# Performance work log

Hardware: AMD Instinct MI355X
Metric: run time of the kernel (lower is better)

The kernel has to match this reference:

```python
import jax, jax.numpy as jnp
import numpy as np

B, T, E, H = 1, 4096, 768, 12
DH = E // H


def setup_inputs() -> dict:
    key = jax.random.key(0)
    ks = jax.random.split(key, 10)
    s = 0.02
    inp = {
        "queries": jax.random.normal(ks[0], (B, T, E), jnp.float32),
        "values": jax.random.normal(ks[1], (B, T, E), jnp.float32),
        # causal mask (1 = keep, 0 = masked), matches masked_fill(mask == 0, -1e9)
        "mask": jnp.tril(jnp.ones((T, T), jnp.int32))[None, None, :, :],
        "Wq": jax.random.normal(ks[2], (E, E), jnp.float32) * s,
        "bq": jnp.zeros((E,), jnp.float32),
        "Wk": jax.random.normal(ks[3], (E, E), jnp.float32) * s,
        "bk": jnp.zeros((E,), jnp.float32),
        "Wv": jax.random.normal(ks[4], (E, E), jnp.float32) * s,
        "bv": jnp.zeros((E,), jnp.float32),
        "Wo": jax.random.normal(ks[5], (E, E), jnp.float32) * s,
        "bo": jnp.zeros((E,), jnp.float32),
    }
    return inp


def _split_heads(x):
    # [B,T,E] -> [B,H,T,DH]
    return x.reshape(B, T, H, DH).transpose(0, 2, 1, 3)


def reference(queries, values, mask, Wq, bq, Wk, bk, Wv, bv, Wo, bo):
    # torch nn.Linear: y = x @ W.T + b
    q = _split_heads(queries @ Wq.T + bq)
    k = _split_heads(values @ Wk.T + bk)
    v = _split_heads(values @ Wv.T + bv)
    scale = 1.0 / np.sqrt(DH).astype(np.float32)
    logits = jnp.einsum("bhqd,bhkd->bhqk", q, k) * scale  # [B,H,T,T]
    logits = jnp.where(mask == 0, jnp.float32(-1e9), logits)
    probs = jax.nn.softmax(logits, axis=-1)
    ctx = jnp.einsum("bhqk,bhkd->bhqd", probs, v)  # [B,H,T,DH]
    ctx = ctx.transpose(0, 2, 1, 3).reshape(B, T, E)
    return ctx @ Wo.T + bo
```

## Files before the change

kernel.cpp:

```cpp
#include <hip/hip_runtime.h>
#include <hip/hip_bf16.h>


typedef __hip_bfloat16 bf16;
typedef __attribute__((ext_vector_type(8))) short short8;
typedef __attribute__((ext_vector_type(4))) short short4v;
typedef __attribute__((ext_vector_type(4))) float f32x4;

#define TSEQ 4096
#define NHEAD 12
#define DHEAD 64
#define EMB 768

#if defined(__HIP_DEVICE_COMPILE__)
#define MFMA16(a, b, c) __builtin_amdgcn_mfma_f32_16x16x16bf16_1k(a, b, c, 0, 0, 0)
#else
#define MFMA16(a, b, c) (c)
#endif

typedef const __attribute__((address_space(1))) unsigned int* gptr_t;
typedef __attribute__((address_space(3))) unsigned int* lptr_t;

__device__ __forceinline__ void load_lds16(const void* g, void* l) {
    __builtin_amdgcn_global_load_lds((gptr_t)g, (lptr_t)l, 16, 0, 0);
}

__device__ __forceinline__ float b2f(short s) {
    unsigned u = ((unsigned)(unsigned short)s) << 16;
    float f;
    __builtin_memcpy(&f, &u, 4);
    return f;
}

__device__ __forceinline__ short f2bs(float f) {
    bf16 h = __float2bfloat16(f);
    short s;
    __builtin_memcpy(&s, &h, 2);
    return s;
}

struct CvtJob { const float* src; bf16* dst; int n; };
struct CvtArgs { CvtJob j[6]; };

__global__ __launch_bounds__(256) void cvt_kernel(CvtArgs a) {
    const CvtJob jb = a.j[blockIdx.y];
    const int i = (blockIdx.x * 256 + threadIdx.x) * 8;
    if (i >= jb.n) return;
    const float4 x0 = *(const float4*)(jb.src + i);
    const float4 x1 = *(const float4*)(jb.src + i + 4);
    bf16 tmp[8];
    tmp[0] = __float2bfloat16(x0.x); tmp[1] = __float2bfloat16(x0.y);
    tmp[2] = __float2bfloat16(x0.z); tmp[3] = __float2bfloat16(x0.w);
    tmp[4] = __float2bfloat16(x1.x); tmp[5] = __float2bfloat16(x1.y);
    tmp[6] = __float2bfloat16(x1.z); tmp[7] = __float2bfloat16(x1.w);
    *(short8*)(jb.dst + i) = *(const short8*)tmp;
}

template<int NF>
__device__ __forceinline__ void gemm_t(
    const bf16* __restrict__ A, const bf16* __restrict__ W,
    const float* __restrict__ bias,
    bf16* __restrict__ outb, float* __restrict__ outf,
    const int mode, const float scale, const int m0, const int n0,
    bf16* sA, bf16* sB)
{
    const int tid  = threadIdx.x;
    const int lane = tid & 63;
    const int wave = tid >> 6;
    const int wr = wave >> 1, wc = wave & 1;
    const int lg = lane >> 4, lr = lane & 15;

    f32x4 acc[4][NF];
#pragma unroll
    for (int m = 0; m < 4; ++m)
#pragma unroll
        for (int n = 0; n < NF; ++n)
            acc[m][n] = (f32x4){0.f, 0.f, 0.f, 0.f};

    for (int k0 = 0; k0 < EMB; k0 += 64) {
        if (k0) __syncthreads();
#pragma unroll
        for (int is = 0; is < 4; ++is) {
            const int chunk = is * 256 + tid;
            const int row = chunk >> 3;
            const int csw = (chunk & 7) ^ (row & 7);
            load_lds16(A + (size_t)(m0 + row) * EMB + k0 + csw * 8,
                       sA + is * 2048 + wave * 512);
        }
#pragma unroll
        for (int is = 0; is < NF; ++is) {
            const int chunk = is * 256 + tid;
            const int row = chunk >> 3;
            const int csw = (chunk & 7) ^ (row & 7);
            load_lds16(W + (size_t)(n0 + row) * EMB + k0 + csw * 8,
                       sB + is * 2048 + wave * 512);
        }
        __syncthreads();

        short8 af[4][2], bfv[NF][2];
#pragma unroll
        for (int m = 0; m < 4; ++m)
#pragma unroll
            for (int kk = 0; kk < 2; ++kk) {
                const int row = wr * 64 + m * 16 + lr;
                const int cc = (kk * 4 + lg) ^ (row & 7);
                af[m][kk] = *(const short8*)(sA + row * 64 + cc * 8);
            }
#pragma unroll
        for (int n = 0; n < NF; ++n)
#pragma unroll
            for (int kk = 0; kk < 2; ++kk) {
                const int row = wc * (NF * 16) + n * 16 + lr;
                const int cc = (kk * 4 + lg) ^ (row & 7);
                bfv[n][kk] = *(const short8*)(sB + row * 64 + cc * 8);
            }
#pragma unroll
        for (int kk = 0; kk < 2; ++kk)
#pragma unroll
            for (int m = 0; m < 4; ++m)
#pragma unroll
                for (int n = 0; n < NF; ++n)
                    acc[m][n] = __builtin_amdgcn_mfma_f32_16x16x32_bf16(
                        af[m][kk], bfv[n][kk], acc[m][n], 0, 0, 0);
    }

#pragma unroll
    for (int n = 0; n < NF; ++n) {
        const int o = n0 + wc * (NF * 16) + n * 16 + lr;
        const float bv = bias[o];
#pragma unroll
        for (int m = 0; m < 4; ++m) {
            const int tbase = m0 + wr * 64 + m * 16 + lg * 4;
#pragma unroll
            for (int r = 0; r < 4; ++r) {
                const float v = (acc[m][n][r] + bv) * scale;
                const int t = tbase + r;
                if (mode == 0)
                    outb[(size_t)(o >> 6) * TSEQ * DHEAD + (size_t)t * DHEAD + (o & 63)] =
                        __float2bfloat16(v);
                else if (mode == 1)
                    outb[(size_t)(o >> 6) * DHEAD * TSEQ + (size_t)(o & 63) * TSEQ + t] =
                        __float2bfloat16(v);
                else
                    outf[(size_t)t * EMB + o] = v;
            }
        }
    }
}

struct QkvArgs {
    const bf16 *xq, *xv, *Wq, *Wk, *Wv;
    const float *bq, *bk, *bv;
    bf16 *qo, *ko, *vto;
};

__global__ __launch_bounds__(256) void qkv_gemm(QkvArgs a) {
    __shared__ __attribute__((aligned(16))) bf16 sA[128 * 64];
    __shared__ __attribute__((aligned(16))) bf16 sB[64 * 64];
    const int z = blockIdx.z;
    const bf16* A = (z == 0) ? a.xq : a.xv;
    const bf16* W = (z == 0) ? a.Wq : (z == 1 ? a.Wk : a.Wv);
    const float* b = (z == 0) ? a.bq : (z == 1 ? a.bk : a.bv);
    bf16* o = (z == 0) ? a.qo : (z == 1 ? a.ko : a.vto);
    const int mode = (z == 2) ? 1 : 0;
    const float scale = (z == 0) ? 0.18033688011112042f : 1.0f;
    gemm_t<2>(A, W, b, o, nullptr, mode, scale, blockIdx.x * 128, blockIdx.y * 64, sA, sB);
}

__global__ __launch_bounds__(256) void out_gemm(
    const bf16* __restrict__ ctx, const bf16* __restrict__ Wo,
    const float* __restrict__ bo, float* __restrict__ out)
{
    __shared__ __attribute__((aligned(16))) bf16 sA[128 * 64];
    __shared__ __attribute__((aligned(16))) bf16 sB[64 * 64];
    gemm_t<2>(ctx, Wo, bo, nullptr, out, 2, 1.0f, blockIdx.x * 128, blockIdx.y * 64, sA, sB);
}

struct AttnState {
    f32x4 O[4];
    float m, l;
};

__device__ __forceinline__ void stage_tile(
    const bf16* __restrict__ Kh, const bf16* __restrict__ Vh,
    bf16* sK, bf16* sV, const int kv0, const int tid)
{
    const int wave = tid >> 6;
#pragma unroll
    for (int is = 0; is < 2; ++is) {
        const int chunk = is * 256 + tid;
        const int row = chunk >> 3;
        const int csw = (chunk & 7) ^ (row & 7);
        load_lds16(Kh + (size_t)(kv0 + row) * DHEAD + csw * 8,
                   sK + is * 2048 + wave * 512);
        load_lds16(Vh + (size_t)row * TSEQ + kv0 + csw * 8,
                   sV + is * 2048 + wave * 512);
    }
}

__device__ __forceinline__ void attn_tile(
    const bf16* sK, const bf16* sV,
    const short8 (&qf)[2], AttnState& st,
    const int kv0, const int qw, const int lane)
{
    const int lg = lane >> 4, lr = lane & 15;
    if (kv0 > qw + 15) return;

    f32x4 s[4];
#pragma unroll
    for (int n = 0; n < 4; ++n) s[n] = (f32x4){0.f, 0.f, 0.f, 0.f};
    short8 kf[4][2];
#pragma unroll
    for (int n = 0; n < 4; ++n)
#pragma unroll
        for (int kk = 0; kk < 2; ++kk) {
            const int row = n * 16 + lr;
            const int cc = (kk * 4 + lg) ^ (row & 7);
            kf[n][kk] = *(const short8*)(sK + row * 64 + cc * 8);
        }
#pragma unroll
    for (int kk = 0; kk < 2; ++kk)
#pragma unroll
        for (int n = 0; n < 4; ++n)
            s[n] = __builtin_amdgcn_mfma_f32_16x16x32_bf16(
                kf[n][kk], qf[kk], s[n], 0, 0, 0);

    if (kv0 + 63 > qw) {
        const int qi = qw + lr;
#pragma unroll
        for (int n = 0; n < 4; ++n) {
            const int kb = kv0 + n * 16 + lg * 4;
#pragma unroll
            for (int r = 0; r < 4; ++r)
                if (kb + r > qi) s[n][r] = -3.0e38f;
        }
    }

    const float a0 = fmaxf(fmaxf(s[0][0], s[0][1]), fmaxf(s[0][2], s[0][3]));
    const float a1 = fmaxf(fmaxf(s[1][0], s[1][1]), fmaxf(s[1][2], s[1][3]));
    const float a2 = fmaxf(fmaxf(s[2][0], s[2][1]), fmaxf(s[2][2], s[2][3]));
    const float a3 = fmaxf(fmaxf(s[3][0], s[3][1]), fmaxf(s[3][2], s[3][3]));
    float mx = fmaxf(fmaxf(a0, a1), fmaxf(a2, a3));
    mx = fmaxf(mx, __shfl_xor(mx, 16));
    mx = fmaxf(mx, __shfl_xor(mx, 32));

    const float mn = fmaxf(st.m, mx);
    const float al = __builtin_amdgcn_exp2f(st.m - mn);
    st.m = mn;

    float rsn[4];
    short4v pq[4];
#pragma unroll
    for (int n = 0; n < 4; ++n) {
        const float p0 = __builtin_amdgcn_exp2f(s[n][0] - mn);
        const float p1 = __builtin_amdgcn_exp2f(s[n][1] - mn);
        const float p2 = __builtin_amdgcn_exp2f(s[n][2] - mn);
        const float p3 = __builtin_amdgcn_exp2f(s[n][3] - mn);
        rsn[n] = (p0 + p1) + (p2 + p3);
        pq[n][0] = f2bs(p0); pq[n][1] = f2bs(p1);
        pq[n][2] = f2bs(p2); pq[n][3] = f2bs(p3);
    }
    float rs = (rsn[0] + rsn[1]) + (rsn[2] + rsn[3]);
    rs += __shfl_xor(rs, 16);
    rs += __shfl_xor(rs, 32);
    st.l = st.l * al + rs;

#pragma unroll
    for (int nd = 0; nd < 4; ++nd)
#pragma unroll
        for (int r = 0; r < 4; ++r)
            st.O[nd][r] *= al;

#pragma unroll
    for (int nd = 0; nd < 4; ++nd) {
        const int row = nd * 16 + lr;
        f32x4 o = st.O[nd];
#pragma unroll
        for (int n = 0; n < 4; ++n) {
            const int c16 = (n * 2 + (lg >> 1)) ^ (row & 7);
            const short4v va = *(const short4v*)(sV + row * 64 + c16 * 8 + (lg & 1) * 4);
            o = MFMA16(va, pq[n], o);
        }
        st.O[nd] = o;
    }
}

__global__ __launch_bounds__(256, 4) void attn_kernel(
    const bf16* __restrict__ Q, const bf16* __restrict__ K,
    const bf16* __restrict__ VT, bf16* __restrict__ Opart,
    float* __restrict__ ml, const int nch_max)
{
    __shared__ __attribute__((aligned(16))) bf16 sK0[64 * 64];
    __shared__ __attribute__((aligned(16))) bf16 sK1[64 * 64];
    __shared__ __attribute__((aligned(16))) bf16 sV0[64 * 64];
    __shared__ __attribute__((aligned(16))) bf16 sV1[64 * 64];

    const int tid  = threadIdx.x;
    const int lane = tid & 63;
    const int wave = tid >> 6;
    const int lg = lane >> 4, lr = lane & 15;
    const int h  = blockIdx.z;
    const int c  = blockIdx.y;
    const int bx = gridDim.x - 1 - blockIdx.x;
    const int q0 = bx * 64;
    const int qw = q0 + wave * 16;

    const int S = bx + 1;
    const int nchb = (nch_max > 1) ? min((S + 5) / 6, nch_max) : 1;
    if (c >= nchb) return;
    const int t0 = (c * S) / nchb;
    const int t1 = ((c + 1) * S) / nchb;

    const bf16* Qh = Q  + (size_t)h * TSEQ * DHEAD;
    const bf16* Kh = K  + (size_t)h * TSEQ * DHEAD;
    const bf16* Vh = VT + (size_t)h * DHEAD * TSEQ;

    short8 qf[2];
#pragma unroll
    for (int kk = 0; kk < 2; ++kk)
        qf[kk] = *(const short8*)(Qh + (size_t)(qw + lr) * DHEAD + kk * 32 + lg * 8);

    AttnState st;
#pragma unroll
    for (int nd = 0; nd < 4; ++nd) st.O[nd] = (f32x4){0.f, 0.f, 0.f, 0.f};
    st.m = -3.0e38f; st.l = 0.f;

    stage_tile(Kh, Vh, sK0, sV0, t0 * 64, tid);
    __syncthreads();

    int it = t0;
    while (it < t1) {
        if (it + 1 < t1) stage_tile(Kh, Vh, sK1, sV1, (it + 1) * 64, tid);
        attn_tile(sK0, sV0, qf, st, it * 64, qw, lane);
        __syncthreads();
        ++it;
        if (it >= t1) break;
        if (it + 1 < t1) stage_tile(Kh, Vh, sK0, sV0, (it + 1) * 64, tid);
        attn_tile(sK1, sV1, qf, st, it * 64, qw, lane);
        __syncthreads();
        ++it;
    }

    const int u = (h * 64 + bx) * nch_max + c;
    bf16* op = Opart + (size_t)u * 4096;
    float* mlp = ml + (size_t)u * 128;
    const int q = wave * 16 + lr;
#pragma unroll
    for (int nd = 0; nd < 4; ++nd) {
        short4v ov;
        ov[0] = f2bs(st.O[nd][0]); ov[1] = f2bs(st.O[nd][1]);
        ov[2] = f2bs(st.O[nd][2]); ov[3] = f2bs(st.O[nd][3]);
        *(short4v*)(op + q * 64 + nd * 16 + lg * 4) = ov;
    }
    if (lg == 0) {
        mlp[q] = st.m;
        mlp[64 + q] = st.l;
    }
}

__global__ __launch_bounds__(256) void combine_kernel(
    const bf16* __restrict__ Opart, const float* __restrict__ ml,
    bf16* __restrict__ ctx, const int nch_max)
{
    const int h  = blockIdx.y;
    const int bx = blockIdx.x;
    const int tid = threadIdx.x;
    const int row = tid >> 2;
    const int dp  = (tid & 3) * 16;
    const int ub = (h * 64 + bx) * nch_max;
    const int S = bx + 1;
    const int nchb = (nch_max > 1) ? min((S + 5) / 6, nch_max) : 1;

    float M = -3.0e38f;
    for (int c = 0; c < nchb; ++c)
        M = fmaxf(M, ml[(size_t)(ub + c) * 128 + row]);

    float L = 0.f;
    float acc[16];
#pragma unroll
    for (int i = 0; i < 16; ++i) acc[i] = 0.f;
    for (int c = 0; c < nchb; ++c) {
        const float mc = ml[(size_t)(ub + c) * 128 + row];
        const float lc = ml[(size_t)(ub + c) * 128 + 64 + row];
        const float w = __builtin_amdgcn_exp2f(mc - M);
        L += lc * w;
        const bf16* op = Opart + ((size_t)(ub + c) * 64 + row) * 64 + dp;
        const short8 v0 = *(const short8*)op;
        const short8 v1 = *(const short8*)(op + 8);
#pragma unroll
        for (int i = 0; i < 8; ++i) acc[i] += w * b2f(v0[i]);
#pragma unroll
        for (int i = 0; i < 8; ++i) acc[8 + i] += w * b2f(v1[i]);
    }
    const float invL = 1.0f / L;

    bf16 outv[16];
#pragma unroll
    for (int i = 0; i < 16; ++i) outv[i] = __float2bfloat16(acc[i] * invL);
    const int t = bx * 64 + row;
    bf16* dst = ctx + (size_t)t * EMB + h * DHEAD + dp;
    *(short8*)dst = *(const short8*)outv;
    *(short8*)(dst + 8) = *(const short8*)(outv + 8);
}

extern "C" void kernel_launch(void* const* d_in, const int* in_sizes, int n_in,
                              void* d_out, int out_size, void* d_ws, size_t ws_size,
                              hipStream_t stream) {
    const float* queries = (const float*)d_in[0];
    const float* values  = (const float*)d_in[1];
    const float* Wq = (const float*)d_in[3];
    const float* bq = (const float*)d_in[4];
    const float* Wk = (const float*)d_in[5];
    const float* bk = (const float*)d_in[6];
    const float* Wv = (const float*)d_in[7];
    const float* bv = (const float*)d_in[8];
    const float* Wo = (const float*)d_in[9];
    const float* bo = (const float*)d_in[10];
    float* out = (float*)d_out;

    const size_t NTE = (size_t)TSEQ * EMB;
    const size_t WSZ = (size_t)EMB * EMB;
    bf16* ws  = (bf16*)d_ws;
    bf16* qb  = ws;
    bf16* vb  = qb + NTE;
    bf16* wqb = vb + NTE;
    bf16* wkb = wqb + WSZ;
    bf16* wvb = wkb + WSZ;
    bf16* wob = wvb + WSZ;
    bf16* qh  = wob + WSZ;
    bf16* kh  = qh + NTE;
    bf16* vth = kh + NTE;
    bf16* ctx = qb;

    const size_t fixed_elems = 5 * NTE + 4 * WSZ;
    int nch = 8;
    for (;;) {
        const size_t units = (size_t)NHEAD * (TSEQ / 64) * nch;
        const size_t need = fixed_elems * 2 + units * 4096 * 2 + units * 128 * 4;
        if (ws_size >= need || nch == 1) break;
        nch = (nch == 8) ? 4 : 1;
    }
    const size_t units = (size_t)NHEAD * (TSEQ / 64) * nch;
    bf16* opart = ws + fixed_elems;
    float* ml = (float*)(opart + units * 4096);

    CvtArgs ca;
    ca.j[0] = {queries, qb,  (int)NTE};
    ca.j[1] = {values,  vb,  (int)NTE};
    ca.j[2] = {Wq,      wqb, (int)WSZ};
    ca.j[3] = {Wk,      wkb, (int)WSZ};
    ca.j[4] = {Wv,      wvb, (int)WSZ};
    ca.j[5] = {Wo,      wob, (int)WSZ};
    cvt_kernel<<<dim3((NTE + 2047) / 2048, 6), 256, 0, stream>>>(ca);

    QkvArgs a{qb, vb, wqb, wkb, wvb, bq, bk, bv, qh, kh, vth};
    qkv_gemm<<<dim3(TSEQ / 128, EMB / 64, 3), 256, 0, stream>>>(a);
    attn_kernel<<<dim3(TSEQ / 64, nch, NHEAD), 256, 0, stream>>>(qh, kh, vth, opart, ml, nch);
    combine_kernel<<<dim3(TSEQ / 64, NHEAD), 256, 0, stream>>>(opart, ml, ctx, nch);
    out_gemm<<<dim3(TSEQ / 128, EMB / 64), 256, 0, stream>>>(ctx, wob, bo, out);
}
```

Baseline: 137.1 us.

## Compact attention grid with group-based split, precompute LDS pointers, widen QKV tile

The attention launch becomes a flat 1D grid of only useful work units. Query blocks are grouped in eights, each group gets a fixed split count, and blocks are ordered so the heaviest ones are scheduled first. This removes the early-exit blocks of the old 3D grid, and the combine kernel uses the same split rule. LDS fragment addresses for K and V are now computed once per thread and indexed with a compile-time buffer offset instead of recomputing swizzled indices each tile. Separately, the QKV GEMM moves to 128-wide N tiles (gemm_t<4>), which halves its block count and doubles its B-tile shared memory.

```diff
diff --git a/kernel.cpp b/kernel.cpp
--- a/kernel.cpp
+++ b/kernel.cpp
@@ -156,7 +156,7 @@
 
 __global__ __launch_bounds__(256) void qkv_gemm(QkvArgs a) {
     __shared__ __attribute__((aligned(16))) bf16 sA[128 * 64];
-    __shared__ __attribute__((aligned(16))) bf16 sB[64 * 64];
+    __shared__ __attribute__((aligned(16))) bf16 sB[128 * 64];
     const int z = blockIdx.z;
     const bf16* A = (z == 0) ? a.xq : a.xv;
     const bf16* W = (z == 0) ? a.Wq : (z == 1 ? a.Wk : a.Wv);
@@ -164,7 +164,7 @@
     bf16* o = (z == 0) ? a.qo : (z == 1 ? a.ko : a.vto);
     const int mode = (z == 2) ? 1 : 0;
     const float scale = (z == 0) ? 0.18033688011112042f : 1.0f;
-    gemm_t<2>(A, W, b, o, nullptr, mode, scale, blockIdx.x * 128, blockIdx.y * 64, sA, sB);
+    gemm_t<4>(A, W, b, o, nullptr, mode, scale, blockIdx.x * 128, blockIdx.y * 128, sA, sB);
 }
 
 __global__ __launch_bounds__(256) void out_gemm(
@@ -198,8 +198,10 @@
     }
 }
 
+template<int BUF>
 __device__ __forceinline__ void attn_tile(
-    const bf16* sK, const bf16* sV,
+    const bf16* kp0, const bf16* kp1,
+    const bf16* vp0, const bf16* vp1, const bf16* vp2, const bf16* vp3,
     const short8 (&qf)[2], AttnState& st,
     const int kv0, const int qw, const int lane)
 {
@@ -207,17 +209,14 @@
     if (kv0 > qw + 15) return;
 
     f32x4 s[4];
+    short8 kf[4][2];
+#pragma unroll
+    for (int n = 0; n < 4; ++n) {
+        kf[n][0] = *(const short8*)(kp0 + BUF * 4096 + n * 1024);
+        kf[n][1] = *(const short8*)(kp1 + BUF * 4096 + n * 1024);
+    }
 #pragma unroll
     for (int n = 0; n < 4; ++n) s[n] = (f32x4){0.f, 0.f, 0.f, 0.f};
-    short8 kf[4][2];
-#pragma unroll
-    for (int n = 0; n < 4; ++n)
-#pragma unroll
-        for (int kk = 0; kk < 2; ++kk) {
-            const int row = n * 16 + lr;
-            const int cc = (kk * 4 + lg) ^ (row & 7);
-            kf[n][kk] = *(const short8*)(sK + row * 64 + cc * 8);
-        }
 #pragma unroll
     for (int kk = 0; kk < 2; ++kk)
 #pragma unroll
@@ -273,14 +272,11 @@
 
 #pragma unroll
     for (int nd = 0; nd < 4; ++nd) {
-        const int row = nd * 16 + lr;
         f32x4 o = st.O[nd];
-#pragma unroll
-        for (int n = 0; n < 4; ++n) {
-            const int c16 = (n * 2 + (lg >> 1)) ^ (row & 7);
-            const short4v va = *(const short4v*)(sV + row * 64 + c16 * 8 + (lg & 1) * 4);
-            o = MFMA16(va, pq[n], o);
-        }
+        o = MFMA16(*(const short4v*)(vp0 + BUF * 4096 + nd * 1024), pq[0], o);
+        o = MFMA16(*(const short4v*)(vp1 + BUF * 4096 + nd * 1024), pq[1], o);
+        o = MFMA16(*(const short4v*)(vp2 + BUF * 4096 + nd * 1024), pq[2], o);
+        o = MFMA16(*(const short4v*)(vp3 + BUF * 4096 + nd * 1024), pq[3], o);
         st.O[nd] = o;
     }
 }
@@ -288,28 +284,36 @@
 __global__ __launch_bounds__(256, 4) void attn_kernel(
     const bf16* __restrict__ Q, const bf16* __restrict__ K,
     const bf16* __restrict__ VT, bf16* __restrict__ Opart,
-    float* __restrict__ ml, const int nch_max)
-{
-    __shared__ __attribute__((aligned(16))) bf16 sK0[64 * 64];
-    __shared__ __attribute__((aligned(16))) bf16 sK1[64 * 64];
-    __shared__ __attribute__((aligned(16))) bf16 sV0[64 * 64];
-    __shared__ __attribute__((aligned(16))) bf16 sV1[64 * 64];
+    float* __restrict__ ml, const int nch_max, const int U)
+{
+    __shared__ __attribute__((aligned(16))) bf16 sK[2][64 * 64];
+    __shared__ __attribute__((aligned(16))) bf16 sV[2][64 * 64];
 
     const int tid  = threadIdx.x;
     const int lane = tid & 63;
     const int wave = tid >> 6;
     const int lg = lane >> 4, lr = lane & 15;
-    const int h  = blockIdx.z;
-    const int c  = blockIdx.y;
-    const int bx = gridDim.x - 1 - blockIdx.x;
+
+    const int bid = blockIdx.x;
+    const int h = bid % 12;
+    int rem = (U - 1) - (bid / 12);
+    int g = 0;
+    while (g < 7) {
+        const int cap = (g + 1 < nch_max) ? g + 1 : nch_max;
+        const int gu = 8 * cap;
+        if (rem < gu) break;
+        rem -= gu;
+        ++g;
+    }
+    const int d = (g + 1 < nch_max) ? g + 1 : nch_max;
+    const int bx = 8 * g + rem / d;
+    const int c = rem % d;
+
     const int q0 = bx * 64;
     const int qw = q0 + wave * 16;
-
     const int S = bx + 1;
-    const int nchb = (nch_max > 1) ? min((S + 5) / 6, nch_max) : 1;
-    if (c >= nchb) return;
-    const int t0 = (c * S) / nchb;
-    const int t1 = ((c + 1) * S) / nchb;
+    const int t0 = (c * S) / d;
+    const int t1 = ((c + 1) * S) / d;
 
     const bf16* Qh = Q  + (size_t)h * TSEQ * DHEAD;
     const bf16* Kh = K  + (size_t)h * TSEQ * DHEAD;
@@ -320,23 +324,33 @@
     for (int kk = 0; kk < 2; ++kk)
         qf[kk] = *(const short8*)(Qh + (size_t)(qw + lr) * DHEAD + kk * 32 + lg * 8);
 
+    const int kb0 = lr * 64 + ((lg ^ (lr & 7)) * 8);
+    const bf16* kp0 = &sK[0][0] + kb0;
+    const bf16* kp1 = &sK[0][0] + (kb0 ^ 32);
+    const int vx = ((lg >> 1) ^ (lr & 7)) * 8;
+    const int vb = lr * 64 + (lg & 1) * 4;
+    const bf16* vp0 = &sV[0][0] + vb + (0 ^ vx);
+    const bf16* vp1 = &sV[0][0] + vb + (16 ^ vx);
+    const bf16* vp2 = &sV[0][0] + vb + (32 ^ vx);
+    const bf16* vp3 = &sV[0][0] + vb + (48 ^ vx);
+
     AttnState st;
 #pragma unroll
     for (int nd = 0; nd < 4; ++nd) st.O[nd] = (f32x4){0.f, 0.f, 0.f, 0.f};
     st.m = -3.0e38f; st.l = 0.f;
 
-    stage_tile(Kh, Vh, sK0, sV0, t0 * 64, tid);
+    stage_tile(Kh, Vh, &sK[0][0], &sV[0][0], t0 * 64, tid);
     __syncthreads();
 
     int it = t0;
     while (it < t1) {
-        if (it + 1 < t1) stage_tile(Kh, Vh, sK1, sV1, (it + 1) * 64, tid);
-        attn_tile(sK0, sV0, qf, st, it * 64, qw, lane);
+        if (it + 1 < t1) stage_tile(Kh, Vh, &sK[1][0], &sV[1][0], (it + 1) * 64, tid);
+        attn_tile<0>(kp0, kp1, vp0, vp1, vp2, vp3, qf, st, it * 64, qw, lane);
         __syncthreads();
         ++it;
         if (it >= t1) break;
-        if (it + 1 < t1) stage_tile(Kh, Vh, sK0, sV0, (it + 1) * 64, tid);
-        attn_tile(sK1, sV1, qf, st, it * 64, qw, lane);
+        if (it + 1 < t1) stage_tile(Kh, Vh, &sK[0][0], &sV[0][0], (it + 1) * 64, tid);
+        attn_tile<1>(kp0, kp1, vp0, vp1, vp2, vp3, qf, st, it * 64, qw, lane);
         __syncthreads();
         ++it;
     }
@@ -368,8 +382,8 @@
     const int row = tid >> 2;
     const int dp  = (tid & 3) * 16;
     const int ub = (h * 64 + bx) * nch_max;
-    const int S = bx + 1;
-    const int nchb = (nch_max > 1) ? min((S + 5) / 6, nch_max) : 1;
+    const int g = bx >> 3;
+    const int nchb = (nch_max > 1) ? ((g + 1 < nch_max) ? g + 1 : nch_max) : 1;
 
     float M = -3.0e38f;
     for (int c = 0; c < nchb; ++c)
@@ -444,6 +458,9 @@
     bf16* opart = ws + fixed_elems;
     float* ml = (float*)(opart + units * 4096);
 
+    int U = 0;
+    for (int g = 0; g < 8; ++g) U += 8 * ((g + 1 < nch) ? g + 1 : nch);
+
     CvtArgs ca;
     ca.j[0] = {queries, qb,  (int)NTE};
     ca.j[1] = {values,  vb,  (int)NTE};
@@ -454,8 +471,8 @@
     cvt_kernel<<<dim3((NTE + 2047) / 2048, 6), 256, 0, stream>>>(ca);
 
     QkvArgs a{qb, vb, wqb, wkb, wvb, bq, bk, bv, qh, kh, vth};
-    qkv_gemm<<<dim3(TSEQ / 128, EMB / 64, 3), 256, 0, stream>>>(a);
-    attn_kernel<<<dim3(TSEQ / 64, nch, NHEAD), 256, 0, stream>>>(qh, kh, vth, opart, ml, nch);
+    qkv_gemm<<<dim3(TSEQ / 128, EMB / 128, 3), 256, 0, stream>>>(a);
+    attn_kernel<<<dim3(12 * U), 256, 0, stream>>>(qh, kh, vth, opart, ml, nch, U);
     combine_kernel<<<dim3(TSEQ / 64, NHEAD), 256, 0, stream>>>(opart, ml, ctx, nch);
     out_gemm<<<dim3(TSEQ / 128, EMB / 64), 256, 0, stream>>>(ctx, wob, bo, out);
 }
```

After: 115.0 us. 1.19x faster.
